# Optimization experiments

Hardware: AMD Instinct MI355X
Metric: run time of the kernel (lower is better)

## Reference

```python
import jax, jax.numpy as jnp
import numpy as np

EPS = 1e-5
K = 7        # deformable/spatial kernel size
GRID = 4     # local pool grid size


def conv(x, w, pad=0):
    # x: NCHW, w: OIHW
    return jax.lax.conv_general_dilated(
        x, w, (1, 1), [(pad, pad), (pad, pad)],
        dimension_numbers=('NCHW', 'OIHW', 'NCHW'))


def bn(x, g, b, m, v):
    # eval-mode batchnorm with running stats
    scale = (g * jax.lax.rsqrt(v + EPS))[None, :, None, None]
    return (x - m[None, :, None, None]) * scale + b[None, :, None, None]


def grid_sample(feat, grid):
    # bilinear, padding_mode='zeros', align_corners=False
    # feat: [b,c,h,w], grid: [b,h,w,2] with (x,y) in [-1,1]
    b, c, h, w = feat.shape
    gx = (grid[..., 0] + 1.0) * (w * 0.5) - 0.5
    gy = (grid[..., 1] + 1.0) * (h * 0.5) - 0.5
    x0 = jnp.floor(gx)
    y0 = jnp.floor(gy)
    wx = gx - x0
    wy = gy - y0
    feat_flat = feat.reshape(b, c, h * w)

    def gather(yi, xi):
        valid = (xi >= 0) & (xi < w) & (yi >= 0) & (yi < h)
        xi_c = jnp.clip(xi, 0, w - 1).astype(jnp.int32)
        yi_c = jnp.clip(yi, 0, h - 1).astype(jnp.int32)
        idx = (yi_c * w + xi_c).reshape(b, 1, h * w)
        vals = jnp.take_along_axis(feat_flat, idx, axis=2).reshape(b, c, h, w)
        return vals * valid[:, None].astype(feat.dtype)

    out = (gather(y0, x0) * ((1 - wx) * (1 - wy))[:, None]
           + gather(y0, x0 + 1) * (wx * (1 - wy))[:, None]
           + gather(y0 + 1, x0) * ((1 - wx) * wy)[:, None]
           + gather(y0 + 1, x0 + 1) * (wx * wy)[:, None])
    return out


def cmife_forward(x, align_w, align_g, align_b, align_m, align_v,
                  mlp_w1, mlp_w2, loc_w1, loc_w2, fusion_w,
                  off_w1, off_g, off_bt, off_m, off_v, off_w2, off_b2,
                  attn_w):
    # ---- align: 1x1 conv + BN + SiLU ----
    x = conv(x, align_w)
    x = bn(x, align_g, align_b, align_m, align_v)
    x = x * jax.nn.sigmoid(x)  # SiLU
    b_, c_, h_, w_ = x.shape

    # ---- LocalGlobalChannelAttention ----
    def mlp(z):
        return conv(jax.nn.relu(conv(z, mlp_w1)), mlp_w2)

    g_avg = mlp(jnp.mean(x, (2, 3), keepdims=True))
    g_max = mlp(jnp.max(x, (2, 3), keepdims=True))
    global_attn = g_avg + g_max
    # adaptive avg pool to GRIDxGRID (h,w divisible by GRID)
    loc = x.reshape(b_, c_, GRID, h_ // GRID, GRID, w_ // GRID).mean((3, 5))
    local_attn = conv(jax.nn.relu(conv(loc, loc_w1)), loc_w2)
    local_attn = local_attn.mean((2, 3), keepdims=True)
    alpha = jax.nn.sigmoid(fusion_w)
    ca = jax.nn.sigmoid(alpha * global_attn + (1 - alpha) * local_attn)
    x = ca * x

    # ---- DeformableSpatialAttention ----
    avg_out = jnp.mean(x, 1, keepdims=True)
    max_out = jnp.max(x, 1, keepdims=True)
    sf = jnp.concatenate([avg_out, max_out], axis=1)  # [b,2,h,w]
    o = jax.nn.relu(bn(conv(sf, off_w1, pad=1), off_g, off_bt, off_m, off_v))
    o = conv(o, off_w2, pad=1) + off_b2[None, :, None, None]  # [b,2*K*K,h,w]
    off = o.reshape(b_, 2, K * K, h_, w_).mean(2)             # [b,2,h,w]
    off = jnp.tanh(off) * 0.5
    off = jnp.transpose(off, (0, 2, 3, 1))                    # [b,h,w,2]
    gy, gx = jnp.meshgrid(jnp.linspace(-1.0, 1.0, h_),
                          jnp.linspace(-1.0, 1.0, w_), indexing='ij')
    base = jnp.stack([gx, gy], axis=-1)[None]                 # [1,h,w,2]
    dgrid = jnp.clip(base + off, -1.0, 1.0)
    sampled = grid_sample(sf, dgrid)                          # [b,2,h,w]
    sa = jax.nn.sigmoid(conv(sampled, attn_w, pad=K // 2))    # [b,1,h,w]
    return sa * x


def setup_inputs() -> dict:
    key = jax.random.key(0)
    ks = jax.random.split(key, 24)
    B, CIN, COUT, H, W, MID = 8, 256, 256, 160, 160, 16
    f = jnp.float32
    inp = {
        'x': jax.random.normal(ks[0], (B, CIN, H, W), f),
        'align_w': jax.random.normal(ks[1], (COUT, CIN, 1, 1), f) * 0.05,
        'align_g': jax.random.uniform(ks[2], (COUT,), f, 0.5, 1.5),
        'align_b': jax.random.normal(ks[3], (COUT,), f) * 0.1,
        'align_m': jax.random.normal(ks[4], (COUT,), f) * 0.1,
        'align_v': jax.random.uniform(ks[5], (COUT,), f, 0.5, 1.5),
        'mlp_w1': jax.random.normal(ks[6], (MID, COUT, 1, 1), f) * 0.1,
        'mlp_w2': jax.random.normal(ks[7], (COUT, MID, 1, 1), f) * 0.1,
        'loc_w1': jax.random.normal(ks[8], (MID, COUT, 1, 1), f) * 0.1,
        'loc_w2': jax.random.normal(ks[9], (COUT, MID, 1, 1), f) * 0.1,
        'fusion_w': jnp.float32(0.5),
        'off_w1': jax.random.normal(ks[10], (16, 2, 3, 3), f) * 0.1,
        'off_g': jax.random.uniform(ks[11], (16,), f, 0.5, 1.5),
        'off_bt': jax.random.normal(ks[12], (16,), f) * 0.1,
        'off_m': jax.random.normal(ks[13], (16,), f) * 0.1,
        'off_v': jax.random.uniform(ks[14], (16,), f, 0.5, 1.5),
        'off_w2': jax.random.normal(ks[15], (2 * K * K, 16, 3, 3), f) * 0.01,
        'off_b2': jax.random.normal(ks[16], (2 * K * K,), f) * 0.01,
        'attn_w': jax.random.normal(ks[17], (1, 2, K, K), f) * 0.1,
    }
    return inp


def reference(x, align_w, align_g, align_b, align_m, align_v,
              mlp_w1, mlp_w2, loc_w1, loc_w2, fusion_w,
              off_w1, off_g, off_bt, off_m, off_v, off_w2, off_b2,
              attn_w):
    return cmife_forward(x, align_w, align_g, align_b, align_m, align_v,
                         mlp_w1, mlp_w2, loc_w1, loc_w2, fusion_w,
                         off_w1, off_g, off_bt, off_m, off_v, off_w2, off_b2,
                         attn_w)
```

## Files before the change

kernel.cpp:

```cpp
#include <hip/hip_runtime.h>
#include <hip/hip_bf16.h>

#define HH 160
#define WW 160
#define HW 25600
#define NC 256
#define NB 8

typedef short short8 __attribute__((ext_vector_type(8)));
typedef float f32x4 __attribute__((ext_vector_type(4)));

__device__ __forceinline__ unsigned short f2bf(float f) {
    unsigned u = __float_as_uint(f);
    u += 0x7fffu + ((u >> 16) & 1u);
    return (unsigned short)(u >> 16);
}
__device__ __forceinline__ float bf2f(unsigned short h) {
    return __uint_as_float(((unsigned)h) << 16);
}

__global__ void k0_fold(const float* __restrict__ aw, const float* __restrict__ ag,
                        const float* __restrict__ ab, const float* __restrict__ am,
                        const float* __restrict__ av,
                        unsigned short* __restrict__ wpkh, unsigned short* __restrict__ wpkl,
                        float* __restrict__ biasp) {
    int co = blockIdx.x, t = threadIdx.x;
    float sc = ag[co] * rsqrtf(av[co] + 1e-5f);
    float w = aw[co * 256 + t] * sc;
    unsigned short h = f2bf(w);
    int kk = t >> 5, kq = t & 31;
    wpkh[kk * 10240 + co * 40 + kq] = h;
    wpkl[kk * 10240 + co * 40 + kq] = f2bf(w - bf2f(h));
    if (t == 0) biasp[co] = ab[co] - am[co] * sc;
}

__global__ void k0b_fold2(const float* __restrict__ ow2, const float* __restrict__ ob2,
                          float* __restrict__ weff, float* __restrict__ beff) {
    int t = threadIdx.x;
    if (t < 288) {
        int g = t / 144, r = t - g * 144;
        float s = 0.f;
        for (int q = 0; q < 49; q++) s += ow2[(size_t)(g * 49 + q) * 144 + r];
        weff[t] = s * (1.f / 49.f);
    }
    if (t < 2) {
        float s = 0.f;
        for (int q = 0; q < 49; q++) s += ob2[t * 49 + q];
        beff[t] = s * (1.f / 49.f);
    }
}

__global__ __launch_bounds__(512, 2) void k1_gemm(
    const float* __restrict__ X, const unsigned short* __restrict__ Wph,
    const unsigned short* __restrict__ Wpl,
    const float* __restrict__ biasp, float* __restrict__ xal) {
    __shared__ __align__(16) unsigned short Ah[10240];
    __shared__ __align__(16) unsigned short Al[10240];
    __shared__ __align__(16) unsigned short Bh[5120];
    __shared__ __align__(16) unsigned short Bl[5120];

    int t = threadIdx.x;
    int n0 = blockIdx.x * 128;
    int b  = blockIdx.y;
    const float* Xb = X + (size_t)b * NC * HW;

    int lane = t & 63, wv = t >> 6;
    int lcol = lane & 15, lq = lane >> 4;

    f32x4 acc[2][8];
#pragma unroll
    for (int i = 0; i < 2; i++)
#pragma unroll
        for (int j = 0; j < 8; j++) { f32x4 z = {0.f, 0.f, 0.f, 0.f}; acc[i][j] = z; }

    int bn  = t & 127;
    int kq2 = t >> 7;

    float pf[8];

    {
        const float* src = Xb + (size_t)(kq2 * 8) * HW + n0 + bn;
#pragma unroll
        for (int j = 0; j < 8; j++) pf[j] = src[(size_t)j * HW];
    }
    {
        const char* gah = (const char*)Wph;
        const char* gal = (const char*)Wpl;
#pragma unroll
        for (int i = 0; i < 3; i++) {
            if (i < 2 || wv < 4) {
                int off = i * 8192 + wv * 1024;
                __builtin_amdgcn_global_load_lds(
                    (const __attribute__((address_space(1))) unsigned int*)(gah + off + lane * 16),
                    (__attribute__((address_space(3))) unsigned int*)((char*)Ah + off),
                    16, 0, 0);
                __builtin_amdgcn_global_load_lds(
                    (const __attribute__((address_space(1))) unsigned int*)(gal + off + lane * 16),
                    (__attribute__((address_space(3))) unsigned int*)((char*)Al + off),
                    16, 0, 0);
            }
        }
    }

    for (int kk = 0; kk < 8; kk++) {
        {
            unsigned hi[4], lo[4];
#pragma unroll
            for (int j = 0; j < 4; j++) {
                unsigned short a = f2bf(pf[2 * j]);
                unsigned short c = f2bf(pf[2 * j + 1]);
                hi[j] = (unsigned)a | ((unsigned)c << 16);
                unsigned short la = f2bf(pf[2 * j] - bf2f(a));
                unsigned short lc = f2bf(pf[2 * j + 1] - bf2f(c));
                lo[j] = (unsigned)la | ((unsigned)lc << 16);
            }
            *(uint4*)(&Bh[bn * 40 + kq2 * 8]) = make_uint4(hi[0], hi[1], hi[2], hi[3]);
            *(uint4*)(&Bl[bn * 40 + kq2 * 8]) = make_uint4(lo[0], lo[1], lo[2], lo[3]);
        }
        __syncthreads();

        short8 afh[2], afl[2];
#pragma unroll
        for (int mt = 0; mt < 2; mt++) {
            afh[mt] = *(const short8*)(&Ah[(wv * 32 + mt * 16 + lcol) * 40 + lq * 8]);
            afl[mt] = *(const short8*)(&Al[(wv * 32 + mt * 16 + lcol) * 40 + lq * 8]);
        }
        if (kk < 7) {
            const float* src = Xb + (size_t)((kk + 1) * 32 + kq2 * 8) * HW + n0 + bn;
#pragma unroll
            for (int j = 0; j < 8; j++) pf[j] = src[(size_t)j * HW];
        }
#pragma unroll
        for (int nt = 0; nt < 8; nt++) {
            short8 bh = *(const short8*)(&Bh[(nt * 16 + lcol) * 40 + lq * 8]);
            short8 bl = *(const short8*)(&Bl[(nt * 16 + lcol) * 40 + lq * 8]);
#pragma unroll
            for (int mt = 0; mt < 2; mt++) {
                acc[mt][nt] = __builtin_amdgcn_mfma_f32_16x16x32_bf16(
                    afh[mt], bh, acc[mt][nt], 0, 0, 0);
                acc[mt][nt] = __builtin_amdgcn_mfma_f32_16x16x32_bf16(
                    afh[mt], bl, acc[mt][nt], 0, 0, 0);
                acc[mt][nt] = __builtin_amdgcn_mfma_f32_16x16x32_bf16(
                    afl[mt], bh, acc[mt][nt], 0, 0, 0);
            }
        }
        asm volatile("s_barrier" ::: "memory");
        if (kk < 7) {
            const char* gah = (const char*)(Wph + (kk + 1) * 10240);
            const char* gal = (const char*)(Wpl + (kk + 1) * 10240);
#pragma unroll
            for (int i = 0; i < 3; i++) {
                if (i < 2 || wv < 4) {
                    int off = i * 8192 + wv * 1024;
                    __builtin_amdgcn_global_load_lds(
                        (const __attribute__((address_space(1))) unsigned int*)(gah + off + lane * 16),
                        (__attribute__((address_space(3))) unsigned int*)((char*)Ah + off),
                        16, 0, 0);
                    __builtin_amdgcn_global_load_lds(
                        (const __attribute__((address_space(1))) unsigned int*)(gal + off + lane * 16),
                        (__attribute__((address_space(3))) unsigned int*)((char*)Al + off),
                        16, 0, 0);
                }
            }
        }
    }
#pragma unroll
    for (int mt = 0; mt < 2; mt++) {
#pragma unroll
        for (int r = 0; r < 4; r++) {
            int co = wv * 32 + mt * 16 + lq * 4 + r;
            float bias = biasp[co];
            size_t rowbase = ((size_t)b * NC + co) * HW + n0;
#pragma unroll
            for (int nt = 0; nt < 8; nt++) {
                int n = nt * 16 + lcol;
                float y = acc[mt][nt][r] + bias;
                float z = y / (1.f + __expf(-y));
                xal[rowbase + n] = z;
            }
        }
    }
}

__global__ void ka_stats(const float* __restrict__ xal,
                         float* __restrict__ cellsum, float* __restrict__ cellmax) {
    __shared__ float rs[320], rm[320];
    int blk = blockIdx.x;
    int bc = blk >> 2, band = blk & 3;
    const float* base = xal + (size_t)bc * HW + band * 6400;
    int t = threadIdx.x;
    int col = (t % 40) / 10;
    float s = 0.f, m = -3.4e38f;
#pragma unroll
    for (int i = 0; i < 5; i++) {
        f32x4 v = *(const f32x4*)(base + (size_t)(i * 320 + t) * 4);
        s += (v[0] + v[1]) + (v[2] + v[3]);
        m = fmaxf(fmaxf(fmaxf(m, v[0]), fmaxf(v[1], v[2])), v[3]);
    }
    int slot = (t / 40) * 10 + (t % 10);
    rs[col * 80 + slot] = s;
    rm[col * 80 + slot] = m;
    __syncthreads();
    if (t < 64) {
#pragma unroll
        for (int c2 = 0; c2 < 4; c2++) {
            float sv = rs[c2 * 80 + t] + ((t < 16) ? rs[c2 * 80 + 64 + t] : 0.f);
            float mv = fmaxf(rm[c2 * 80 + t],
                             (t < 16) ? rm[c2 * 80 + 64 + t] : -3.4e38f);
#pragma unroll
            for (int off = 32; off >= 1; off >>= 1) {
                sv += __shfl_down(sv, off, 64);
                mv = fmaxf(mv, __shfl_down(mv, off, 64));
            }
            if (t == 0) {
                cellsum[bc * 16 + band * 4 + c2] = sv;
                cellmax[bc * 16 + band * 4 + c2] = mv;
            }
        }
    }
}

__global__ void kb_attn(const float* __restrict__ cellsum, const float* __restrict__ cellmax,
                        const float* __restrict__ mw1, const float* __restrict__ mw2,
                        const float* __restrict__ lw1, const float* __restrict__ lw2,
                        const float* __restrict__ fw, float* __restrict__ ca) {
    __shared__ float avgS[256], maxS[256], locS[256 * 16], hid[32], hlS[256];
    int b = blockIdx.x, t = threadIdx.x;
    float s = 0.f, m = -3.4e38f;
#pragma unroll
    for (int cell = 0; cell < 16; cell++) {
        float cs = cellsum[(b * 256 + t) * 16 + cell];
        float cm = cellmax[(b * 256 + t) * 16 + cell];
        s += cs;
        m = fmaxf(m, cm);
        locS[t * 16 + cell] = cs * (1.f / 1600.f);
    }
    avgS[t] = s * (1.f / 25600.f);
    maxS[t] = m;
    __syncthreads();
    if (t < 32) {
        int j = t & 15;
        const float* w1 = mw1 + j * 256;
        const float* src = (t < 16) ? avgS : maxS;
        float h = 0.f;
        for (int c = 0; c < 256; c++) h += w1[c] * src[c];
        hid[t] = fmaxf(h, 0.f);
    }
    {
        int cell = t >> 4, j = t & 15;
        const float* w1 = lw1 + j * 256;
        float h = 0.f;
        for (int c = 0; c < 256; c++) h += w1[c] * locS[c * 16 + cell];
        hlS[t] = fmaxf(h, 0.f);
    }
    __syncthreads();
    float ga = 0.f, gm = 0.f;
#pragma unroll
    for (int j = 0; j < 16; j++) {
        float w2 = mw2[t * 16 + j];
        ga += w2 * hid[j];
        gm += w2 * hid[16 + j];
    }
    float la = 0.f;
#pragma unroll
    for (int cell = 0; cell < 16; cell++)
#pragma unroll
        for (int j = 0; j < 16; j++)
            la += lw2[t * 16 + j] * hlS[cell * 16 + j];
    float alpha = 1.f / (1.f + expf(-fw[0]));
    float pre = alpha * (ga + gm) + (1.f - alpha) * (la * (1.f / 16.f));
    ca[b * 256 + t] = 1.f / (1.f + expf(-pre));
}

__global__ void k3_sf(const float* __restrict__ xal,
                      const float* __restrict__ ca, float* __restrict__ sf) {
    __shared__ float cas[256];
    int b = blockIdx.y, t = threadIdx.x;
    cas[t] = ca[b * 256 + t];
    __syncthreads();
    int p = blockIdx.x * 256 + t;
    const float* base = xal + (size_t)b * NC * HW + p;
    float s0 = 0.f, m0 = -3.4e38f;
    for (int c = 0; c < 256; c++) {
        float a0 = cas[c] * base[(size_t)c * HW];
        s0 += a0;
        m0 = fmaxf(m0, a0);
    }
    sf[(size_t)b * 2 * HW + p]      = s0 * (1.f / 256.f);
    sf[(size_t)b * 2 * HW + HW + p] = m0;
}

__global__ void k45_sample(const float* __restrict__ sf, const float* __restrict__ ow1,
                           const float* __restrict__ og, const float* __restrict__ obt,
                           const float* __restrict__ om, const float* __restrict__ ov,
                           const float* __restrict__ weff, const float* __restrict__ beff,
                           float* __restrict__ sampled) {
    __shared__ float sfS[800];
    __shared__ float tileS[16 * 18 * 18];
    __shared__ float w1S[288], scS[16], shS[16];
    __shared__ float wS[288];
    __shared__ float bS[2];
    int b = blockIdx.y, t = threadIdx.x;
    int ty0 = (blockIdx.x / 10) * 16, tx0 = (blockIdx.x % 10) * 16;
    const float* f0 = sf + (size_t)b * 2 * HW;
    const float* f1 = f0 + HW;
    for (int i = t; i < 288; i += 256) { w1S[i] = ow1[i]; wS[i] = weff[i]; }
    if (t < 16) {
        float sc = og[t] * rsqrtf(ov[t] + 1e-5f);
        scS[t] = sc;
        shS[t] = obt[t] - om[t] * sc;
    }
    if (t < 2) bS[t] = beff[t];
    for (int i = t; i < 800; i += 256) {
        int ch = i / 400, rem = i - ch * 400;
        int r = rem / 20, c = rem - r * 20;
        int gr = ty0 + r - 2, gc = tx0 + c - 2;
        bool ok = (gr >= 0) & (gr < 160) & (gc >= 0) & (gc < 160);
        sfS[i] = ok ? f0[(size_t)ch * HW + gr * 160 + gc] : 0.f;
    }
    __syncthreads();
    for (int i = t; i < 16 * 324; i += 256) {
        int ci = i / 324, rem = i - ci * 324;
        int r = rem / 18, c = rem - r * 18;
        int gr = ty0 + r - 1, gc = tx0 + c - 1;
        float acc = 0.f;
#pragma unroll
        for (int kh = 0; kh < 3; kh++)
#pragma unroll
            for (int kw = 0; kw < 3; kw++) {
                int k = kh * 3 + kw;
                acc += w1S[ci * 18 + k]     * sfS[(r + kh) * 20 + (c + kw)]
                     + w1S[ci * 18 + 9 + k] * sfS[400 + (r + kh) * 20 + (c + kw)];
            }
        bool ok = (gr >= 0) & (gr < 160) & (gc >= 0) & (gc < 160);
        tileS[i] = ok ? fmaxf(acc * scS[ci] + shS[ci], 0.f) : 0.f;
    }
    __syncthreads();
    int ty = t >> 4, tx = t & 15;
    int h = ty0 + ty, w = tx0 + tx;
    int p = h * 160 + w;
    float s0 = bS[0], s1 = bS[1];
#pragma unroll
    for (int ci = 0; ci < 16; ci++) {
        const float* tb = &tileS[ci * 324 + ty * 18 + tx];
        const float* w0 = &wS[ci * 9];
        const float* w1 = &wS[144 + ci * 9];
#pragma unroll
        for (int kh = 0; kh < 3; kh++)
#pragma unroll
            for (int kw = 0; kw < 3; kw++) {
                float v = tb[kh * 18 + kw];
                s0 += w0[kh * 3 + kw] * v;
                s1 += w1[kh * 3 + kw] * v;
            }
    }
    float ox = tanhf(s0) * 0.5f;
    float oy = tanhf(s1) * 0.5f;
    float bx = w * (2.f / 159.f) - 1.f, by = h * (2.f / 159.f) - 1.f;
    float gxn = fminf(fmaxf(bx + ox, -1.f), 1.f);
    float gyn = fminf(fmaxf(by + oy, -1.f), 1.f);
    float gx = (gxn + 1.f) * 80.f - 0.5f;
    float gy = (gyn + 1.f) * 80.f - 0.5f;
    float x0f = floorf(gx), y0f = floorf(gy);
    float wx = gx - x0f, wy = gy - y0f;
    int ix0 = (int)x0f, iy0 = (int)y0f;
    float r0 = 0.f, r1 = 0.f;
#pragma unroll
    for (int dy = 0; dy < 2; dy++)
#pragma unroll
        for (int dx = 0; dx < 2; dx++) {
            int xi = ix0 + dx, yi = iy0 + dy;
            float wgt = (dx ? wx : 1.f - wx) * (dy ? wy : 1.f - wy);
            if ((xi >= 0) & (xi < 160) & (yi >= 0) & (yi < 160)) {
                int q = yi * 160 + xi;
                r0 += wgt * f0[q];
                r1 += wgt * f1[q];
            }
        }
    float* sb = sampled + (size_t)b * 2 * HW + p;
    sb[0] = r0;
    sb[HW] = r1;
}

__global__ void k5b_sa(const float* __restrict__ sampled, const float* __restrict__ attn_w,
                       float* __restrict__ sa) {
    __shared__ float wS[98];
    int b = blockIdx.y, t = threadIdx.x;
    if (t < 98) wS[t] = attn_w[t];
    __syncthreads();
    int p = blockIdx.x * 256 + t;
    int h = p / 160, w = p - h * 160;
    const float* s0 = sampled + (size_t)b * 2 * HW;
    const float* s1 = s0 + HW;
    float acc = 0.f;
#pragma unroll
    for (int kh = 0; kh < 7; kh++) {
        int hh = h + kh - 3;
        if (hh < 0 || hh >= 160) continue;
#pragma unroll
        for (int kw = 0; kw < 7; kw++) {
            int ww = w + kw - 3;
            if (ww < 0 || ww >= 160) continue;
            int q = hh * 160 + ww;
            acc += wS[kh * 7 + kw] * s0[q] + wS[49 + kh * 7 + kw] * s1[q];
        }
    }
    sa[(size_t)b * HW + p] = 1.f / (1.f + expf(-acc));
}

__global__ void k6_out(float* __restrict__ out, const float* __restrict__ ca,
                       const float* __restrict__ sa) {
    unsigned e4 = blockIdx.x * 256 + threadIdx.x;
    unsigned e = e4 * 4;
    unsigned b = e / (256u * HW);
    unsigned rem = e - b * (256u * HW);
    unsigned c = rem / HW;
    unsigned p = rem - c * HW;
    f32x4 v = *(f32x4*)(out + e);
    f32x4 s = *(const f32x4*)(sa + (size_t)b * HW + p);
    float cav = ca[b * 256 + c];
#pragma unroll
    for (int i = 0; i < 4; i++) v[i] = cav * s[i] * v[i];
    *(f32x4*)(out + e) = v;
}

extern "C" void kernel_launch(void* const* d_in, const int* in_sizes, int n_in,
                              void* d_out, int out_size, void* d_ws, size_t ws_size,
                              hipStream_t stream) {
    const float* x       = (const float*)d_in[0];
    const float* align_w = (const float*)d_in[1];
    const float* align_g = (const float*)d_in[2];
    const float* align_b = (const float*)d_in[3];
    const float* align_m = (const float*)d_in[4];
    const float* align_v = (const float*)d_in[5];
    const float* mlp_w1  = (const float*)d_in[6];
    const float* mlp_w2  = (const float*)d_in[7];
    const float* loc_w1  = (const float*)d_in[8];
    const float* loc_w2  = (const float*)d_in[9];
    const float* fusion  = (const float*)d_in[10];
    const float* off_w1  = (const float*)d_in[11];
    const float* off_g   = (const float*)d_in[12];
    const float* off_bt  = (const float*)d_in[13];
    const float* off_m   = (const float*)d_in[14];
    const float* off_v   = (const float*)d_in[15];
    const float* off_w2  = (const float*)d_in[16];
    const float* off_b2  = (const float*)d_in[17];
    const float* attn_w  = (const float*)d_in[18];
    float* out = (float*)d_out;

    char* wsb = (char*)d_ws;
    size_t off = 0;
    auto alloc = [&](size_t bytes) -> void* {
        off = (off + 255) & ~(size_t)255;
        void* p = wsb + off;
        off += bytes;
        return p;
    };
    float* xal = out;
    unsigned short* wph = (unsigned short*)alloc(81920 * 2);
    unsigned short* wpl = (unsigned short*)alloc(81920 * 2);
    float* biasp   = (float*)alloc(256 * 4);
    float* cellsum = (float*)alloc(32768 * 4);
    float* cellmax = (float*)alloc(32768 * 4);
    float* ca      = (float*)alloc(2048 * 4);
    float* sf      = (float*)alloc((size_t)NB * 2 * HW * 4);
    float* sampled = (float*)alloc((size_t)NB * 2 * HW * 4);
    float* sa      = (float*)alloc((size_t)NB * HW * 4);
    float* weff    = (float*)alloc(288 * 4);
    float* beff    = (float*)alloc(2 * 4);
    (void)ws_size; (void)in_sizes; (void)n_in; (void)out_size;

    k0_fold<<<dim3(256), 256, 0, stream>>>(align_w, align_g, align_b, align_m, align_v,
                                           wph, wpl, biasp);
    k0b_fold2<<<dim3(1), 320, 0, stream>>>(off_w2, off_b2, weff, beff);
    k1_gemm<<<dim3(200, 8), 512, 0, stream>>>(x, wph, wpl, biasp, xal);
    ka_stats<<<dim3(8192), 320, 0, stream>>>(xal, cellsum, cellmax);
    kb_attn<<<dim3(8), 256, 0, stream>>>(cellsum, cellmax, mlp_w1, mlp_w2,
                                         loc_w1, loc_w2, fusion, ca);
    k3_sf<<<dim3(100, 8), 256, 0, stream>>>(xal, ca, sf);
    k45_sample<<<dim3(100, 8), 256, 0, stream>>>(sf, off_w1, off_g, off_bt, off_m, off_v,
                                                 weff, beff, sampled);
    k5b_sa<<<dim3(100, 8), 256, 0, stream>>>(sampled, attn_w, sa);
    k6_out<<<dim3(51200), 256, 0, stream>>>(out, ca, sa);
}
```

Before: 706.0 us.

## Retile GEMM to 4 waves, vectorize channel reduction, tile 7x7 conv in LDS

```diff
diff --git a/kernel.cpp b/kernel.cpp
--- a/kernel.cpp
+++ b/kernel.cpp
@@ -50,7 +50,7 @@
     }
 }
 
-__global__ __launch_bounds__(512, 2) void k1_gemm(
+__global__ __launch_bounds__(256, 2) void k1_gemm(
     const float* __restrict__ X, const unsigned short* __restrict__ Wph,
     const unsigned short* __restrict__ Wpl,
     const float* __restrict__ biasp, float* __restrict__ xal) {
@@ -67,29 +67,108 @@
     int lane = t & 63, wv = t >> 6;
     int lcol = lane & 15, lq = lane >> 4;
 
-    f32x4 acc[2][8];
-#pragma unroll
-    for (int i = 0; i < 2; i++)
+    f32x4 acc[4][8];
+#pragma unroll
+    for (int i = 0; i < 4; i++)
 #pragma unroll
         for (int j = 0; j < 8; j++) { f32x4 z = {0.f, 0.f, 0.f, 0.f}; acc[i][j] = z; }
 
-    int bn  = t & 127;
-    int kq2 = t >> 7;
-
-    float pf[8];
-
-    {
-        const float* src = Xb + (size_t)(kq2 * 8) * HW + n0 + bn;
-#pragma unroll
-        for (int j = 0; j < 8; j++) pf[j] = src[(size_t)j * HW];
+    int bn2 = t & 63;
+    int bkq = t >> 6;
+
+    float2 pf[8];
+
+#pragma unroll
+    for (int j2 = 0; j2 < 2; j2++) {
+        int kq = bkq + 4 * j2;
+        const float* src = Xb + (size_t)(kq * 4) * HW + n0 + bn2 * 2;
+#pragma unroll
+        for (int j = 0; j < 2; j++) {
+            pf[j2 * 4 + 2 * j]     = *(const float2*)(src + (size_t)(2 * j) * HW);
+            pf[j2 * 4 + 2 * j + 1] = *(const float2*)(src + (size_t)(2 * j + 1) * HW);
+        }
     }
     {
         const char* gah = (const char*)Wph;
         const char* gal = (const char*)Wpl;
 #pragma unroll
-        for (int i = 0; i < 3; i++) {
-            if (i < 2 || wv < 4) {
-                int off = i * 8192 + wv * 1024;
+        for (int i = 0; i < 5; i++) {
+            int off = wv * 1024 + i * 4096;
+            __builtin_amdgcn_global_load_lds(
+                (const __attribute__((address_space(1))) unsigned int*)(gah + off + lane * 16),
+                (__attribute__((address_space(3))) unsigned int*)((char*)Ah + off),
+                16, 0, 0);
+            __builtin_amdgcn_global_load_lds(
+                (const __attribute__((address_space(1))) unsigned int*)(gal + off + lane * 16),
+                (__attribute__((address_space(3))) unsigned int*)((char*)Al + off),
+                16, 0, 0);
+        }
+    }
+
+    for (int kk = 0; kk < 8; kk++) {
+#pragma unroll
+        for (int j2 = 0; j2 < 2; j2++) {
+            int kq = bkq + 4 * j2;
+            unsigned h0[2], h1[2], l0[2], l1[2];
+#pragma unroll
+            for (int j = 0; j < 2; j++) {
+                float2 v0 = pf[j2 * 4 + 2 * j];
+                float2 v1 = pf[j2 * 4 + 2 * j + 1];
+                unsigned short a = f2bf(v0.x), bq = f2bf(v1.x);
+                unsigned short c = f2bf(v0.y), d = f2bf(v1.y);
+                h0[j] = (unsigned)a | ((unsigned)bq << 16);
+                h1[j] = (unsigned)c | ((unsigned)d << 16);
+                unsigned short la = f2bf(v0.x - bf2f(a)), lb = f2bf(v1.x - bf2f(bq));
+                unsigned short lc = f2bf(v0.y - bf2f(c)), ld = f2bf(v1.y - bf2f(d));
+                l0[j] = (unsigned)la | ((unsigned)lb << 16);
+                l1[j] = (unsigned)lc | ((unsigned)ld << 16);
+            }
+            *(uint2*)(&Bh[(bn2 * 2) * 40 + kq * 4])     = make_uint2(h0[0], h0[1]);
+            *(uint2*)(&Bh[(bn2 * 2 + 1) * 40 + kq * 4]) = make_uint2(h1[0], h1[1]);
+            *(uint2*)(&Bl[(bn2 * 2) * 40 + kq * 4])     = make_uint2(l0[0], l0[1]);
+            *(uint2*)(&Bl[(bn2 * 2 + 1) * 40 + kq * 4]) = make_uint2(l1[0], l1[1]);
+        }
+        __syncthreads();
+
+        short8 afh[4], afl[4];
+#pragma unroll
+        for (int mt = 0; mt < 4; mt++) {
+            afh[mt] = *(const short8*)(&Ah[(wv * 64 + mt * 16 + lcol) * 40 + lq * 8]);
+            afl[mt] = *(const short8*)(&Al[(wv * 64 + mt * 16 + lcol) * 40 + lq * 8]);
+        }
+        if (kk < 7) {
+#pragma unroll
+            for (int j2 = 0; j2 < 2; j2++) {
+                int kq = bkq + 4 * j2;
+                const float* src = Xb + (size_t)((kk + 1) * 32 + kq * 4) * HW + n0 + bn2 * 2;
+#pragma unroll
+                for (int j = 0; j < 2; j++) {
+                    pf[j2 * 4 + 2 * j]     = *(const float2*)(src + (size_t)(2 * j) * HW);
+                    pf[j2 * 4 + 2 * j + 1] = *(const float2*)(src + (size_t)(2 * j + 1) * HW);
+                }
+            }
+        }
+#pragma unroll
+        for (int nt = 0; nt < 8; nt++) {
+            short8 bh = *(const short8*)(&Bh[(nt * 16 + lcol) * 40 + lq * 8]);
+            short8 bl = *(const short8*)(&Bl[(nt * 16 + lcol) * 40 + lq * 8]);
+#pragma unroll
+            for (int mt = 0; mt < 4; mt++) {
+                acc[mt][nt] = __builtin_amdgcn_mfma_f32_16x16x32_bf16(
+                    afh[mt], bh, acc[mt][nt], 0, 0, 0);
+                acc[mt][nt] = __builtin_amdgcn_mfma_f32_16x16x32_bf16(
+                    afh[mt], bl, acc[mt][nt], 0, 0, 0);
+                acc[mt][nt] = __builtin_amdgcn_mfma_f32_16x16x32_bf16(
+                    afl[mt], bh, acc[mt][nt], 0, 0, 0);
+            }
+        }
+        asm volatile("s_barrier" ::: "memory");
+        if (kk < 7) {
+            const char* gah = (const char*)(Wph + (kk + 1) * 10240);
+            const char* gal = (const char*)(Wpl + (kk + 1) * 10240);
+#pragma unroll
+            for (int i = 0; i < 5; i++) {
+                int off = wv * 1024 + i * 4096;
                 __builtin_amdgcn_global_load_lds(
                     (const __attribute__((address_space(1))) unsigned int*)(gah + off + lane * 16),
                     (__attribute__((address_space(3))) unsigned int*)((char*)Ah + off),
@@ -101,74 +180,11 @@
             }
         }
     }
-
-    for (int kk = 0; kk < 8; kk++) {
-        {
-            unsigned hi[4], lo[4];
-#pragma unroll
-            for (int j = 0; j < 4; j++) {
-                unsigned short a = f2bf(pf[2 * j]);
-                unsigned short c = f2bf(pf[2 * j + 1]);
-                hi[j] = (unsigned)a | ((unsigned)c << 16);
-                unsigned short la = f2bf(pf[2 * j] - bf2f(a));
-                unsigned short lc = f2bf(pf[2 * j + 1] - bf2f(c));
-                lo[j] = (unsigned)la | ((unsigned)lc << 16);
-            }
-            *(uint4*)(&Bh[bn * 40 + kq2 * 8]) = make_uint4(hi[0], hi[1], hi[2], hi[3]);
-            *(uint4*)(&Bl[bn * 40 + kq2 * 8]) = make_uint4(lo[0], lo[1], lo[2], lo[3]);
-        }
-        __syncthreads();
-
-        short8 afh[2], afl[2];
-#pragma unroll
-        for (int mt = 0; mt < 2; mt++) {
-            afh[mt] = *(const short8*)(&Ah[(wv * 32 + mt * 16 + lcol) * 40 + lq * 8]);
-            afl[mt] = *(const short8*)(&Al[(wv * 32 + mt * 16 + lcol) * 40 + lq * 8]);
-        }
-        if (kk < 7) {
-            const float* src = Xb + (size_t)((kk + 1) * 32 + kq2 * 8) * HW + n0 + bn;
-#pragma unroll
-            for (int j = 0; j < 8; j++) pf[j] = src[(size_t)j * HW];
-        }
-#pragma unroll
-        for (int nt = 0; nt < 8; nt++) {
-            short8 bh = *(const short8*)(&Bh[(nt * 16 + lcol) * 40 + lq * 8]);
-            short8 bl = *(const short8*)(&Bl[(nt * 16 + lcol) * 40 + lq * 8]);
-#pragma unroll
-            for (int mt = 0; mt < 2; mt++) {
-                acc[mt][nt] = __builtin_amdgcn_mfma_f32_16x16x32_bf16(
-                    afh[mt], bh, acc[mt][nt], 0, 0, 0);
-                acc[mt][nt] = __builtin_amdgcn_mfma_f32_16x16x32_bf16(
-                    afh[mt], bl, acc[mt][nt], 0, 0, 0);
-                acc[mt][nt] = __builtin_amdgcn_mfma_f32_16x16x32_bf16(
-                    afl[mt], bh, acc[mt][nt], 0, 0, 0);
-            }
-        }
-        asm volatile("s_barrier" ::: "memory");
-        if (kk < 7) {
-            const char* gah = (const char*)(Wph + (kk + 1) * 10240);
-            const char* gal = (const char*)(Wpl + (kk + 1) * 10240);
-#pragma unroll
-            for (int i = 0; i < 3; i++) {
-                if (i < 2 || wv < 4) {
-                    int off = i * 8192 + wv * 1024;
-                    __builtin_amdgcn_global_load_lds(
-                        (const __attribute__((address_space(1))) unsigned int*)(gah + off + lane * 16),
-                        (__attribute__((address_space(3))) unsigned int*)((char*)Ah + off),
-                        16, 0, 0);
-                    __builtin_amdgcn_global_load_lds(
-                        (const __attribute__((address_space(1))) unsigned int*)(gal + off + lane * 16),
-                        (__attribute__((address_space(3))) unsigned int*)((char*)Al + off),
-                        16, 0, 0);
-                }
-            }
-        }
-    }
-#pragma unroll
-    for (int mt = 0; mt < 2; mt++) {
+#pragma unroll
+    for (int mt = 0; mt < 4; mt++) {
 #pragma unroll
         for (int r = 0; r < 4; r++) {
-            int co = wv * 32 + mt * 16 + lq * 4 + r;
+            int co = wv * 64 + mt * 16 + lq * 4 + r;
             float bias = biasp[co];
             size_t rowbase = ((size_t)b * NC + co) * HW + n0;
 #pragma unroll
@@ -278,16 +294,24 @@
     int b = blockIdx.y, t = threadIdx.x;
     cas[t] = ca[b * 256 + t];
     __syncthreads();
-    int p = blockIdx.x * 256 + t;
+    int p = (blockIdx.x * 256 + t) * 4;
     const float* base = xal + (size_t)b * NC * HW + p;
-    float s0 = 0.f, m0 = -3.4e38f;
+    f32x4 s = {0.f, 0.f, 0.f, 0.f};
+    f32x4 m = {-3.4e38f, -3.4e38f, -3.4e38f, -3.4e38f};
     for (int c = 0; c < 256; c++) {
-        float a0 = cas[c] * base[(size_t)c * HW];
-        s0 += a0;
-        m0 = fmaxf(m0, a0);
-    }
-    sf[(size_t)b * 2 * HW + p]      = s0 * (1.f / 256.f);
-    sf[(size_t)b * 2 * HW + HW + p] = m0;
+        f32x4 v = *(const f32x4*)(base + (size_t)c * HW);
+        float cav = cas[c];
+#pragma unroll
+        for (int i = 0; i < 4; i++) {
+            float a0 = cav * v[i];
+            s[i] += a0;
+            m[i] = fmaxf(m[i], a0);
+        }
+    }
+#pragma unroll
+    for (int i = 0; i < 4; i++) s[i] *= (1.f / 256.f);
+    *(f32x4*)(sf + (size_t)b * 2 * HW + p)      = s;
+    *(f32x4*)(sf + (size_t)b * 2 * HW + HW + p) = m;
 }
 
 __global__ void k45_sample(const float* __restrict__ sf, const float* __restrict__ ow1,
@@ -384,28 +408,31 @@
 
 __global__ void k5b_sa(const float* __restrict__ sampled, const float* __restrict__ attn_w,
                        float* __restrict__ sa) {
-    __shared__ float wS[98];
+    __shared__ float s0S[484], s1S[484], wS[98];
     int b = blockIdx.y, t = threadIdx.x;
+    int ty0 = (blockIdx.x / 10) * 16, tx0 = (blockIdx.x % 10) * 16;
     if (t < 98) wS[t] = attn_w[t];
-    __syncthreads();
-    int p = blockIdx.x * 256 + t;
-    int h = p / 160, w = p - h * 160;
     const float* s0 = sampled + (size_t)b * 2 * HW;
     const float* s1 = s0 + HW;
+    for (int i = t; i < 484; i += 256) {
+        int r = i / 22, c = i - r * 22;
+        int gr = ty0 + r - 3, gc = tx0 + c - 3;
+        bool ok = (gr >= 0) & (gr < 160) & (gc >= 0) & (gc < 160);
+        int q = gr * 160 + gc;
+        s0S[i] = ok ? s0[q] : 0.f;
+        s1S[i] = ok ? s1[q] : 0.f;
+    }
+    __syncthreads();
+    int ty = t >> 4, tx = t & 15;
     float acc = 0.f;
 #pragma unroll
-    for (int kh = 0; kh < 7; kh++) {
-        int hh = h + kh - 3;
-        if (hh < 0 || hh >= 160) continue;
+    for (int kh = 0; kh < 7; kh++)
 #pragma unroll
         for (int kw = 0; kw < 7; kw++) {
-            int ww = w + kw - 3;
-            if (ww < 0 || ww >= 160) continue;
-            int q = hh * 160 + ww;
-            acc += wS[kh * 7 + kw] * s0[q] + wS[49 + kh * 7 + kw] * s1[q];
-        }
-    }
-    sa[(size_t)b * HW + p] = 1.f / (1.f + expf(-acc));
+            int q = (ty + kh) * 22 + (tx + kw);
+            acc += wS[kh * 7 + kw] * s0S[q] + wS[49 + kh * 7 + kw] * s1S[q];
+        }
+    sa[(size_t)b * HW + (ty0 + ty) * 160 + tx0 + tx] = 1.f / (1.f + expf(-acc));
 }
 
 __global__ void k6_out(float* __restrict__ out, const float* __restrict__ ca,
@@ -473,11 +500,11 @@
     k0_fold<<<dim3(256), 256, 0, stream>>>(align_w, align_g, align_b, align_m, align_v,
                                            wph, wpl, biasp);
     k0b_fold2<<<dim3(1), 320, 0, stream>>>(off_w2, off_b2, weff, beff);
-    k1_gemm<<<dim3(200, 8), 512, 0, stream>>>(x, wph, wpl, biasp, xal);
+    k1_gemm<<<dim3(200, 8), 256, 0, stream>>>(x, wph, wpl, biasp, xal);
     ka_stats<<<dim3(8192), 320, 0, stream>>>(xal, cellsum, cellmax);
     kb_attn<<<dim3(8), 256, 0, stream>>>(cellsum, cellmax, mlp_w1, mlp_w2,
                                          loc_w1, loc_w2, fusion, ca);
-    k3_sf<<<dim3(100, 8), 256, 0, stream>>>(xal, ca, sf);
+    k3_sf<<<dim3(25, 8), 256, 0, stream>>>(xal, ca, sf);
     k45_sample<<<dim3(100, 8), 256, 0, stream>>>(sf, off_w1, off_g, off_bt, off_m, off_v,
                                                  weff, beff, sampled);
     k5b_sa<<<dim3(100, 8), 256, 0, stream>>>(sampled, attn_w, sa);
```

Result: faster. 668.8 us (-5.3%).
